# Performance work log

Measured on AMD Instinct MI355X. Metric: run time of the kernel, lower is better.

The kernel has to match this reference:

```python
import jax, jax.numpy as jnp
import numpy as np

B = 1024          # batch
N_COLS = 8192     # input feature dim
N_ROWS = 8192     # output feature dim (unique values in ij[:,0])
NNZ_PER_ROW = 32
NNZ = N_ROWS * NNZ_PER_ROW


def setup_inputs() -> dict:
    key = jax.random.key(0)
    k1, k2, k3 = jax.random.split(key, 3)
    inputs = jax.random.normal(k1, (B, N_COLS), dtype=jnp.float32)
    sparse_kernel = jax.random.normal(k2, (NNZ, 1), dtype=jnp.float32)
    # ij[:,0] sorted with every row present (matches np.unique/split in __init__)
    rows = jnp.repeat(jnp.arange(N_ROWS, dtype=jnp.int64), NNZ_PER_ROW)
    cols = jax.random.randint(k3, (NNZ,), 0, N_COLS, dtype=jnp.int64)
    return {"inputs": inputs, "sparse_kernel": sparse_kernel,
            "rows": rows, "cols": cols}


def reference(inputs, sparse_kernel, rows, cols):
    # For each nnz entry k: contribution = inputs[:, cols[k]] * sparse_kernel[k]
    # accumulated into output row rows[k].  Equivalent to inputs @ W_sparse^T.
    gathered = inputs.T[cols] * sparse_kernel          # (nnz, B)
    out = jax.ops.segment_sum(gathered, rows, num_segments=N_ROWS)  # (n_rows, B)
    return out.T                                       # (B, n_rows)
```

## Files before the change

### kernel.cpp

```cpp
#include <hip/hip_runtime.h>

#define BATCH 1024
#define NCOLS 8192
#define NROWS 8192
#define NNZPR 32
#define BT3   128
#define RB3   32
#define TS    132

__device__ __forceinline__ uint f2bf(float f) {
    uint u = __float_as_uint(f);
    return (u + 0x7fffu + ((u >> 16) & 1u)) >> 16;
}

template <int N> __device__ __forceinline__ void vm_wait() {
    static_assert(N >= 0 && N <= 15, "");
    if      constexpr (N == 0)  asm volatile("s_waitcnt vmcnt(0)"  ::: "memory");
    else if constexpr (N == 1)  asm volatile("s_waitcnt vmcnt(1)"  ::: "memory");
    else if constexpr (N == 2)  asm volatile("s_waitcnt vmcnt(2)"  ::: "memory");
    else if constexpr (N == 3)  asm volatile("s_waitcnt vmcnt(3)"  ::: "memory");
    else if constexpr (N == 4)  asm volatile("s_waitcnt vmcnt(4)"  ::: "memory");
    else if constexpr (N == 5)  asm volatile("s_waitcnt vmcnt(5)"  ::: "memory");
    else if constexpr (N == 6)  asm volatile("s_waitcnt vmcnt(6)"  ::: "memory");
    else if constexpr (N == 7)  asm volatile("s_waitcnt vmcnt(7)"  ::: "memory");
    else if constexpr (N == 8)  asm volatile("s_waitcnt vmcnt(8)"  ::: "memory");
    else if constexpr (N == 9)  asm volatile("s_waitcnt vmcnt(9)"  ::: "memory");
    else if constexpr (N == 10) asm volatile("s_waitcnt vmcnt(10)" ::: "memory");
    else if constexpr (N == 11) asm volatile("s_waitcnt vmcnt(11)" ::: "memory");
    else if constexpr (N == 12) asm volatile("s_waitcnt vmcnt(12)" ::: "memory");
    else if constexpr (N == 13) asm volatile("s_waitcnt vmcnt(13)" ::: "memory");
    else if constexpr (N == 14) asm volatile("s_waitcnt vmcnt(14)" ::: "memory");
    else                        asm volatile("s_waitcnt vmcnt(15)" ::: "memory");
}

__global__ __launch_bounds__(256) void transpose_bf16(const float* __restrict__ x,
                                                      uint* __restrict__ xth) {
    __shared__ float tile[64][65];
    const int c0 = blockIdx.x * 64;
    const int b0 = blockIdx.y * 64;
    const int t  = threadIdx.x;
    const int tx = t & 63;
    const int ty = t >> 6;

#pragma unroll
    for (int i = 0; i < 16; ++i) {
        const int b = ty + i * 4;
        tile[b][tx] = x[(size_t)(b0 + b) * NCOLS + c0 + tx];
    }
    __syncthreads();

    const int tx2 = t & 31;
    const int h   = t >> 5;
#pragma unroll
    for (int i = 0; i < 8; ++i) {
        const int c = h + i * 8;
        const uint lo = f2bf(tile[2 * tx2 + 0][c]);
        const uint hi = f2bf(tile[2 * tx2 + 1][c]);
        xth[(size_t)(c0 + c) * (BATCH / 2) + (b0 >> 1) + tx2] = lo | (hi << 16);
    }
}

#define FMAB(L, VF) do {                                     \
    ax += __uint_as_float((L).x << 16) * (VF);               \
    ay += __uint_as_float((L).x & 0xffff0000u) * (VF);       \
    az += __uint_as_float((L).y << 16) * (VF);               \
    aw += __uint_as_float((L).y & 0xffff0000u) * (VF);       \
} while (0)

#define ISSUE(i, off)                                        \
    asm volatile("global_load_dwordx2 %0, %1, %2"            \
                 : "=v"(dat[i]) : "v"(off), "s"(sbase))

#define DRAIN(i, n) do {                                     \
    vm_wait<n>(); __builtin_amdgcn_sched_barrier(0);         \
    FMAB(dat[i], vv[i]);                                     \
} while (0)

__global__ __launch_bounds__(256) void spmm_v10(const ushort* __restrict__ xth,
                                                const float* __restrict__ vals,
                                                const int*   __restrict__ cols,
                                                float* __restrict__ out) {
    __shared__ __align__(16) char smem[RB3 * TS * 2 + RB3 * NNZPR * 8];
    ushort* tile   = (ushort*)smem;
    int2*   s_pair = (int2*)(smem + RB3 * TS * 2);

    const int bid = blockIdx.x;
    const int bt  = bid & 7;
    const int rt  = bid >> 3;
    const int t   = threadIdx.x;

    const int nnzbase = rt * RB3 * NNZPR;
    for (int i = t; i < RB3 * NNZPR; i += 256) {
        int2 p;
        p.x = cols[nnzbase + i] << 11;
        p.y = __float_as_int(vals[nnzbase + i]);
        s_pair[i] = p;
    }
    __syncthreads();

    const int hw  = t >> 5;
    const int sl  = t & 31;
    const uint slb = (uint)sl * 8;
    const ushort* sbase = xth + bt * BT3;

#pragma unroll 1
    for (int pass = 0; pass < 4; ++pass) {
        const int row = pass * 8 + hw;
        const int4* mrow = (const int4*)(s_pair + row * NNZPR);

        uint2 dat[32];
        float vv[32];
        float ax = 0.f, ay = 0.f, az = 0.f, aw = 0.f;

#pragma unroll
        for (int j = 0; j < 8; ++j) {
            const int4 m = mrow[j];
            vv[2 * j]     = __int_as_float(m.y);
            vv[2 * j + 1] = __int_as_float(m.w);
            const uint o0 = (uint)m.x + slb;
            const uint o1 = (uint)m.z + slb;
            ISSUE(2 * j,     o0);
            ISSUE(2 * j + 1, o1);
        }

#pragma unroll
        for (int j = 8; j < 16; ++j) {
            const int4 m = mrow[j];
            const uint o0 = (uint)m.x + slb;
            const uint o1 = (uint)m.z + slb;
            vv[2 * j]     = __int_as_float(m.y);
            vv[2 * j + 1] = __int_as_float(m.w);

            vm_wait<15>(); __builtin_amdgcn_sched_barrier(0);
            FMAB(dat[2 * (j - 8)], vv[2 * (j - 8)]);
            ISSUE(2 * j, o0);

            vm_wait<15>(); __builtin_amdgcn_sched_barrier(0);
            FMAB(dat[2 * (j - 8) + 1], vv[2 * (j - 8) + 1]);
            ISSUE(2 * j + 1, o1);
        }

        DRAIN(16, 15); DRAIN(17, 14); DRAIN(18, 13); DRAIN(19, 12);
        DRAIN(20, 11); DRAIN(21, 10); DRAIN(22,  9); DRAIN(23,  8);
        DRAIN(24,  7); DRAIN(25,  6); DRAIN(26,  5); DRAIN(27,  4);
        DRAIN(28,  3); DRAIN(29,  2); DRAIN(30,  1); DRAIN(31,  0);

        const uint u0 = f2bf(ax) | (f2bf(ay) << 16);
        const uint u1 = f2bf(az) | (f2bf(aw) << 16);
        *(uint2*)&tile[row * TS + sl * 4] = make_uint2(u0, u1);
    }
    __syncthreads();

    const int rr = t & 31;
    const int bq = t >> 5;
    const size_t obase = (size_t)(bt * BT3) * NROWS + (size_t)(rt * RB3);
#pragma unroll
    for (int p = 0; p < 16; ++p) {
        const int b = p * 8 + bq;
        out[obase + (size_t)b * NROWS + rr] =
            __uint_as_float((uint)tile[rr * TS + b] << 16);
    }
}

__global__ __launch_bounds__(256) void spmm_fallback(const float* __restrict__ x,
                                                     const float* __restrict__ vals,
                                                     const int*   __restrict__ cols,
                                                     float* __restrict__ out) {
    __shared__ __align__(16) char smem[64 * 65 * 4];
    int*   s_col = (int*)smem;
    float* s_val = (float*)(smem + 64 * 32 * 4);

    const int bid  = blockIdx.x;
    const int bt   = bid & 15;
    const int rt   = bid >> 4;
    const int t    = threadIdx.x;
    const int lane = t & 63;
    const int wave = t >> 6;

    const int nnzbase = rt * 64 * NNZPR;
    for (int i = t; i < 64 * NNZPR; i += 256) {
        s_col[i] = cols[nnzbase + i];
        s_val[i] = vals[nnzbase + i];
    }
    __syncthreads();

    const int b = bt * 64 + lane;
    const float* __restrict__ xb = x + (size_t)b * NCOLS;

    const int rbase = wave * 16;
    float acc[16];
#pragma unroll
    for (int i = 0; i < 16; ++i) acc[i] = 0.f;

    for (int i = 0; i < 16; ++i) {
        const int p = (rbase + i) * NNZPR;
        float a = 0.f;
#pragma unroll
        for (int k = 0; k < NNZPR; ++k)
            a += xb[s_col[p + k]] * s_val[p + k];
        acc[i] = a;
    }
    __syncthreads();

    float* tile = (float*)smem;
#pragma unroll
    for (int i = 0; i < 16; ++i)
        tile[lane * 65 + rbase + i] = acc[i];
    __syncthreads();

    const int rl  = t & 63;
    const int bl0 = t >> 6;
    const size_t obase = (size_t)(bt * 64) * NROWS + (size_t)rt * 64;
#pragma unroll
    for (int p = 0; p < 16; ++p) {
        const int bl = bl0 + p * 4;
        out[obase + (size_t)bl * NROWS + rl] = tile[bl * 65 + rl];
    }
}

extern "C" void kernel_launch(void* const* d_in, const int* in_sizes, int n_in,
                              void* d_out, int out_size, void* d_ws, size_t ws_size,
                              hipStream_t stream) {
    const float* x    = (const float*)d_in[0];
    const float* vals = (const float*)d_in[1];
    const int*   cols = (const int*)d_in[3];
    float* out = (float*)d_out;

    const size_t xth_bytes = (size_t)NCOLS * BATCH * sizeof(ushort);
    if (ws_size >= xth_bytes) {
        uint* xth = (uint*)d_ws;
        dim3 tgrid(NCOLS / 64, BATCH / 64);
        transpose_bf16<<<tgrid, 256, 0, stream>>>(x, xth);
        spmm_v10<<<(NROWS / RB3) * (BATCH / BT3), 256, 0, stream>>>(
            (const ushort*)xth, vals, cols, out);
    } else {
        spmm_fallback<<<(NROWS / 64) * (BATCH / 64), 256, 0, stream>>>(
            x, vals, cols, out);
    }
}
```

Before: 50.14 us.

## Widen gather loads to dwordx4 with 16 lanes per row and padded metadata

New measurement: 41.68 us. 16.9% less time.

```diff
diff --git a/kernel.cpp b/kernel.cpp
--- a/kernel.cpp
+++ b/kernel.cpp
@@ -6,7 +6,8 @@
 #define NNZPR 32
 #define BT3   128
 #define RB3   32
-#define TS    132
+#define MS    33
+#define TS    136
 
 __device__ __forceinline__ uint f2bf(float f) {
     uint u = __float_as_uint(f);
@@ -22,15 +23,7 @@
     else if constexpr (N == 4)  asm volatile("s_waitcnt vmcnt(4)"  ::: "memory");
     else if constexpr (N == 5)  asm volatile("s_waitcnt vmcnt(5)"  ::: "memory");
     else if constexpr (N == 6)  asm volatile("s_waitcnt vmcnt(6)"  ::: "memory");
-    else if constexpr (N == 7)  asm volatile("s_waitcnt vmcnt(7)"  ::: "memory");
-    else if constexpr (N == 8)  asm volatile("s_waitcnt vmcnt(8)"  ::: "memory");
-    else if constexpr (N == 9)  asm volatile("s_waitcnt vmcnt(9)"  ::: "memory");
-    else if constexpr (N == 10) asm volatile("s_waitcnt vmcnt(10)" ::: "memory");
-    else if constexpr (N == 11) asm volatile("s_waitcnt vmcnt(11)" ::: "memory");
-    else if constexpr (N == 12) asm volatile("s_waitcnt vmcnt(12)" ::: "memory");
-    else if constexpr (N == 13) asm volatile("s_waitcnt vmcnt(13)" ::: "memory");
-    else if constexpr (N == 14) asm volatile("s_waitcnt vmcnt(14)" ::: "memory");
-    else                        asm volatile("s_waitcnt vmcnt(15)" ::: "memory");
+    else                        asm volatile("s_waitcnt vmcnt(7)"  ::: "memory");
 }
 
 __global__ __launch_bounds__(256) void transpose_bf16(const float* __restrict__ x,
@@ -60,29 +53,33 @@
     }
 }
 
-#define FMAB(L, VF) do {                                     \
-    ax += __uint_as_float((L).x << 16) * (VF);               \
-    ay += __uint_as_float((L).x & 0xffff0000u) * (VF);       \
-    az += __uint_as_float((L).y << 16) * (VF);               \
-    aw += __uint_as_float((L).y & 0xffff0000u) * (VF);       \
+#define FMA8(D, VF) do {                                     \
+    a0 += __uint_as_float((D).x << 16) * (VF);               \
+    a1 += __uint_as_float((D).x & 0xffff0000u) * (VF);       \
+    a2 += __uint_as_float((D).y << 16) * (VF);               \
+    a3 += __uint_as_float((D).y & 0xffff0000u) * (VF);       \
+    a4 += __uint_as_float((D).z << 16) * (VF);               \
+    a5 += __uint_as_float((D).z & 0xffff0000u) * (VF);       \
+    a6 += __uint_as_float((D).w << 16) * (VF);               \
+    a7 += __uint_as_float((D).w & 0xffff0000u) * (VF);       \
 } while (0)
 
-#define ISSUE(i, off)                                        \
-    asm volatile("global_load_dwordx2 %0, %1, %2"            \
+#define ISSUE4(i, off)                                       \
+    asm volatile("global_load_dwordx4 %0, %1, %2"            \
                  : "=v"(dat[i]) : "v"(off), "s"(sbase))
 
 #define DRAIN(i, n) do {                                     \
     vm_wait<n>(); __builtin_amdgcn_sched_barrier(0);         \
-    FMAB(dat[i], vv[i]);                                     \
+    FMA8(dat[i], vv[i]);                                     \
 } while (0)
 
-__global__ __launch_bounds__(256) void spmm_v10(const ushort* __restrict__ xth,
+__global__ __launch_bounds__(256) void spmm_v11(const ushort* __restrict__ xth,
                                                 const float* __restrict__ vals,
                                                 const int*   __restrict__ cols,
                                                 float* __restrict__ out) {
-    __shared__ __align__(16) char smem[RB3 * TS * 2 + RB3 * NNZPR * 8];
-    ushort* tile   = (ushort*)smem;
-    int2*   s_pair = (int2*)(smem + RB3 * TS * 2);
+    __shared__ __align__(16) char smem[RB3 * MS * 8 + RB3 * TS * 2];
+    int2*   s_pair = (int2*)smem;
+    ushort* tile   = (ushort*)(smem + RB3 * MS * 8);
 
     const int bid = blockIdx.x;
     const int bt  = bid & 7;
@@ -94,60 +91,49 @@
         int2 p;
         p.x = cols[nnzbase + i] << 11;
         p.y = __float_as_int(vals[nnzbase + i]);
-        s_pair[i] = p;
-    }
-    __syncthreads();
-
-    const int hw  = t >> 5;
-    const int sl  = t & 31;
-    const uint slb = (uint)sl * 8;
+        s_pair[(i >> 5) * MS + (i & 31)] = p;
+    }
+    __syncthreads();
+
+    const int wv   = t >> 6;
+    const int qw   = (t >> 4) & 3;
+    const int sl16 = t & 15;
+    const uint slb = (uint)sl16 * 16;
     const ushort* sbase = xth + bt * BT3;
 
 #pragma unroll 1
-    for (int pass = 0; pass < 4; ++pass) {
-        const int row = pass * 8 + hw;
-        const int4* mrow = (const int4*)(s_pair + row * NNZPR);
-
-        uint2 dat[32];
+    for (int qp = 0; qp < 2; ++qp) {
+        const int row = wv * 8 + qp * 4 + qw;
+        const int2* mrow = s_pair + row * MS;
+
+        uint4 dat[32];
         float vv[32];
-        float ax = 0.f, ay = 0.f, az = 0.f, aw = 0.f;
+        float a0 = 0.f, a1 = 0.f, a2 = 0.f, a3 = 0.f;
+        float a4 = 0.f, a5 = 0.f, a6 = 0.f, a7 = 0.f;
 
 #pragma unroll
         for (int j = 0; j < 8; ++j) {
-            const int4 m = mrow[j];
-            vv[2 * j]     = __int_as_float(m.y);
-            vv[2 * j + 1] = __int_as_float(m.w);
-            const uint o0 = (uint)m.x + slb;
-            const uint o1 = (uint)m.z + slb;
-            ISSUE(2 * j,     o0);
-            ISSUE(2 * j + 1, o1);
+            const int2 m = mrow[j];
+            vv[j] = __int_as_float(m.y);
+            ISSUE4(j, (uint)m.x + slb);
         }
-
-#pragma unroll
-        for (int j = 8; j < 16; ++j) {
-            const int4 m = mrow[j];
-            const uint o0 = (uint)m.x + slb;
-            const uint o1 = (uint)m.z + slb;
-            vv[2 * j]     = __int_as_float(m.y);
-            vv[2 * j + 1] = __int_as_float(m.w);
-
-            vm_wait<15>(); __builtin_amdgcn_sched_barrier(0);
-            FMAB(dat[2 * (j - 8)], vv[2 * (j - 8)]);
-            ISSUE(2 * j, o0);
-
-            vm_wait<15>(); __builtin_amdgcn_sched_barrier(0);
-            FMAB(dat[2 * (j - 8) + 1], vv[2 * (j - 8) + 1]);
-            ISSUE(2 * j + 1, o1);
+#pragma unroll
+        for (int j = 8; j < 32; ++j) {
+            const int2 m = mrow[j];
+            vv[j] = __int_as_float(m.y);
+            const uint off = (uint)m.x + slb;
+            vm_wait<7>(); __builtin_amdgcn_sched_barrier(0);
+            FMA8(dat[j - 8], vv[j - 8]);
+            ISSUE4(j, off);
         }
-
-        DRAIN(16, 15); DRAIN(17, 14); DRAIN(18, 13); DRAIN(19, 12);
-        DRAIN(20, 11); DRAIN(21, 10); DRAIN(22,  9); DRAIN(23,  8);
-        DRAIN(24,  7); DRAIN(25,  6); DRAIN(26,  5); DRAIN(27,  4);
-        DRAIN(28,  3); DRAIN(29,  2); DRAIN(30,  1); DRAIN(31,  0);
-
-        const uint u0 = f2bf(ax) | (f2bf(ay) << 16);
-        const uint u1 = f2bf(az) | (f2bf(aw) << 16);
-        *(uint2*)&tile[row * TS + sl * 4] = make_uint2(u0, u1);
+        DRAIN(24, 7); DRAIN(25, 6); DRAIN(26, 5); DRAIN(27, 4);
+        DRAIN(28, 3); DRAIN(29, 2); DRAIN(30, 1); DRAIN(31, 0);
+
+        const uint u0 = f2bf(a0) | (f2bf(a1) << 16);
+        const uint u1 = f2bf(a2) | (f2bf(a3) << 16);
+        const uint u2 = f2bf(a4) | (f2bf(a5) << 16);
+        const uint u3 = f2bf(a6) | (f2bf(a7) << 16);
+        *(uint4*)&tile[row * TS + sl16 * 8] = make_uint4(u0, u1, u2, u3);
     }
     __syncthreads();
 
@@ -231,7 +217,7 @@
         uint* xth = (uint*)d_ws;
         dim3 tgrid(NCOLS / 64, BATCH / 64);
         transpose_bf16<<<tgrid, 256, 0, stream>>>(x, xth);
-        spmm_v10<<<(NROWS / RB3) * (BATCH / BT3), 256, 0, stream>>>(
+        spmm_v11<<<(NROWS / RB3) * (BATCH / BT3), 256, 0, stream>>>(
             (const ushort*)xth, vals, cols, out);
     } else {
         spmm_fallback<<<(NROWS / 64) * (BATCH / 64), 256, 0, stream>>>(
```
